# Optimization experiments

Hardware: AMD Instinct MI355X
Metric: run time of the kernel (lower is better)

The kernel has to match this reference:

```python
import jax, jax.numpy as jnp
from jax import lax
import numpy as np

N_VOX = 50000
B = 2
D, H, W = 8, 160, 160
CIN = 16
G = 3
K = 27
CHANS = [(16, 16), (16, 32), (32, 64), (64, 64), (64, 128)]
NAMES = ['in', 'e1', 'e2', 'e3', 'out']


def setup_inputs() -> dict:
    key = jax.random.key(0)
    ks = jax.random.split(key, 16)
    rng = np.random.default_rng(0)
    # unique active cells -> deterministic scatter/gather rulebook
    lin = rng.choice(B * D * H * W, size=N_VOX, replace=False)
    bz = lin // (D * H * W)
    rem = lin % (D * H * W)
    zz = rem // (H * W)
    yy = (rem % (H * W)) // W
    xx = rem % W
    coors = jnp.asarray(np.stack([bz, zz, yy, xx], 1).astype(np.int32))
    inp = {
        'voxel_features': jax.random.normal(ks[0], (N_VOX, CIN), jnp.float32),
        'coors': coors,
        'batch_size': B,
    }
    i = 1
    for nm, (ci, co) in zip(NAMES, CHANS):
        k1, k2 = jax.random.split(ks[i]); i += 1
        inp['wb_' + nm] = jax.random.normal(k1, (K, ci, co), jnp.float32) * 0.05
        inp['ws_' + nm] = jax.random.normal(k2, (K, ci, G, co), jnp.float32) * 0.05
        inp['gm_' + nm] = jnp.ones((co,), jnp.float32)
        inp['bt_' + nm] = jnp.zeros((co,), jnp.float32)
    return inp


def _kan_block(feat, nbr, wb, ws, gm, bt, centers, inv_h):
    # submanifold KAN conv: gather -> (silu base + RBF spline basis) GEMM -> accumulate
    n = feat.shape[0]
    fp = jnp.concatenate([feat, jnp.zeros((1, feat.shape[1]), feat.dtype)], 0)  # pad row for out-of-grid

    def body(acc, kin):
        idx, wbk, wsk = kin
        x = fp[idx]                                   # [N, Cin] gathered neighbors
        base = jax.nn.silu(x) @ wbk                   # [N, Cout]
        bas = jnp.exp(-jnp.square((x[:, :, None] - centers) * inv_h))  # [N, Cin, G]
        spl = jnp.einsum('ncg,cgo->no', bas, wsk)     # [N, Cout]
        return acc + base + spl, None

    out0 = jnp.zeros((n, wb.shape[-1]), feat.dtype)
    out, _ = lax.scan(jax.checkpoint(body), out0, (nbr, wb, ws))
    # BatchNorm1d (train-mode batch stats) + ReLU
    mu = out.mean(0)
    var = out.var(0)
    out = (out - mu) * lax.rsqrt(var + 1e-3) * gm + bt
    return jax.nn.relu(out)


def _build_rulebook(coors, batch_size, n):
    grid = jnp.full((batch_size, D + 2, H + 2, W + 2), n, jnp.int32)
    grid = grid.at[coors[:, 0], coors[:, 1] + 1, coors[:, 2] + 1, coors[:, 3] + 1].set(
        jnp.arange(n, dtype=jnp.int32))
    offs = [(dz, dy, dx) for dz in (-1, 0, 1) for dy in (-1, 0, 1) for dx in (-1, 0, 1)]
    return jnp.stack([
        grid[coors[:, 0], coors[:, 1] + 1 + dz, coors[:, 2] + 1 + dy, coors[:, 3] + 1 + dx]
        for dz, dy, dx in offs])  # [27, N]


def reference(voxel_features, coors, batch_size,
              wb_in, ws_in, gm_in, bt_in,
              wb_e1, ws_e1, gm_e1, bt_e1,
              wb_e2, ws_e2, gm_e2, bt_e2,
              wb_e3, ws_e3, gm_e3, bt_e3,
              wb_out, ws_out, gm_out, bt_out):
    n = voxel_features.shape[0]
    nbr = _build_rulebook(coors, batch_size, n)
    centers = jnp.linspace(-1.0, 1.0, G)
    inv_h = (G - 1) / 2.0
    x = _kan_block(voxel_features, nbr, wb_in, ws_in, gm_in, bt_in, centers, inv_h)
    x = _kan_block(x, nbr, wb_e1, ws_e1, gm_e1, bt_e1, centers, inv_h)
    x = _kan_block(x, nbr, wb_e2, ws_e2, gm_e2, bt_e2, centers, inv_h)
    x = _kan_block(x, nbr, wb_e3, ws_e3, gm_e3, bt_e3, centers, inv_h)
    x = _kan_block(x, nbr, wb_out, ws_out, gm_out, bt_out, centers, inv_h)
    co = x.shape[1]
    dense = jnp.zeros((batch_size, D, H, W, co), x.dtype)
    dense = dense.at[coors[:, 0], coors[:, 1], coors[:, 2], coors[:, 3]].set(x)
    dense = dense.transpose(0, 4, 1, 2, 3)            # [B, C, D, H, W]
    return dense.reshape(batch_size, co * D, H, W)    # [B, C*D, H, W]
```

## Files before the change

### kernel.cpp

```cpp
#include <hip/hip_runtime.h>

#define N_VOX 50000
#define BATCH 2
#define DD 8
#define HH 160
#define WW 160
#define PD 10
#define PH 162
#define PW 162
#define KK 27
#define NCELL (BATCH*DD*HH*WW)
#define GRID_ELEMS (BATCH*PD*PH*PW)
#define OUT_ELEMS (BATCH*128*DD*HH*WW)

typedef __attribute__((ext_vector_type(8))) short short8v;
typedef __attribute__((ext_vector_type(4))) float float4v;

__device__ inline unsigned short f2bf(float f) {
    unsigned u = __float_as_uint(f);
    u += 0x7FFFu + ((u >> 16) & 1u);
    return (unsigned short)(u >> 16);
}

__global__ void k_flags(const int* __restrict__ coors, int* __restrict__ flags) {
    int n = blockIdx.x * 256 + threadIdx.x;
    if (n >= N_VOX) return;
    int b = coors[n*4+0], z = coors[n*4+1], y = coors[n*4+2], x = coors[n*4+3];
    flags[((b*DD + z)*HH + y)*WW + x] = 1;
}

__global__ void k_scan1(const int* __restrict__ flags, int* __restrict__ scanout,
                        int* __restrict__ bsums) {
    __shared__ int s[256];
    int t = threadIdx.x, blk = blockIdx.x;
    int4 v = ((const int4*)(flags + blk*1024))[t];
    int tsum = v.x + v.y + v.z + v.w;
    s[t] = tsum; __syncthreads();
    for (int off = 1; off < 256; off <<= 1) {
        int x = (t >= off) ? s[t-off] : 0;
        __syncthreads(); s[t] += x; __syncthreads();
    }
    int excl = s[t] - tsum;
    int4 o; o.x = excl; o.y = excl + v.x; o.z = o.y + v.y; o.w = o.z + v.z;
    ((int4*)(scanout + blk*1024))[t] = o;
    if (t == 255) bsums[blk] = s[255];
}

__global__ void k_scan2(int* __restrict__ bsums) {
    __shared__ int s[512];
    int t = threadIdx.x;
    int orig = (t < 400) ? bsums[t] : 0;
    s[t] = orig; __syncthreads();
    for (int off = 1; off < 512; off <<= 1) {
        int x = (t >= off) ? s[t-off] : 0;
        __syncthreads(); s[t] += x; __syncthreads();
    }
    if (t < 400) bsums[t] = s[t] - orig;
}

__global__ void k_pos(const int* __restrict__ coors, const int* __restrict__ scanout,
                      const int* __restrict__ bsums, int* __restrict__ pos_of,
                      int* __restrict__ vox_at) {
    int n = blockIdx.x * 256 + threadIdx.x;
    if (n >= N_VOX) return;
    int b = coors[n*4+0], z = coors[n*4+1], y = coors[n*4+2], x = coors[n*4+3];
    int lin = ((b*DD + z)*HH + y)*WW + x;
    int pos = scanout[lin] + bsums[lin >> 10];
    pos_of[n] = pos;
    vox_at[pos] = n;
}

__global__ void k_gridP(const int* __restrict__ coors, const int* __restrict__ pos_of,
                        int* __restrict__ gridP) {
    int n = blockIdx.x * 256 + threadIdx.x;
    if (n >= N_VOX) return;
    int b = coors[n*4+0], z = coors[n*4+1], y = coors[n*4+2], x = coors[n*4+3];
    gridP[((b*PD + z+1)*PH + (y+1))*PW + (x+1)] = pos_of[n];
}

__global__ void k_nbrP(const int* __restrict__ coors, const int* __restrict__ vox_at,
                       const int* __restrict__ gridP, int* __restrict__ nbrP) {
    int i = blockIdx.x * 256 + threadIdx.x;
    if (i >= N_VOX) return;
    int n = vox_at[i];
    int b = coors[n*4+0], z = coors[n*4+1]+1, y = coors[n*4+2]+1, x = coors[n*4+3]+1;
    int k = 0;
    for (int dz = -1; dz <= 1; ++dz)
        for (int dy = -1; dy <= 1; ++dy)
            for (int dx = -1; dx <= 1; ++dx) {
                int g = gridP[((b*PD + z+dz)*PH + (y+dy))*PW + (x+dx)];
                nbrP[k*N_VOX + i] = (g >= 0) ? g : N_VOX;
                ++k;
            }
}

__global__ void k_phi0(const float* __restrict__ vf, const int* __restrict__ vox_at,
                       unsigned short* __restrict__ phi) {
    int e = blockIdx.x * 256 + threadIdx.x;
    if (e >= (N_VOX + 1) * 16) return;
    int i = e / 16, c = e % 16;
    float x = 0.f;
    if (i < N_VOX) x = vf[(size_t)vox_at[i] * 16 + c];
    float sig = 1.f / (1.f + __expf(-x));
    ushort4 p;
    p.x = f2bf(x * sig);
    p.y = f2bf(__expf(-(x + 1.f) * (x + 1.f)));
    p.z = f2bf(__expf(-x * x));
    p.w = f2bf(__expf(-(x - 1.f) * (x - 1.f)));
    *(ushort4*)&phi[(size_t)e * 4] = p;
}

struct WswzArgs {
    const float* wb[5];
    const float* ws[5];
    unsigned short* dst[5];
};
__global__ void k_wswz_all(WswzArgs a) {
    constexpr int off[6]   = {0, 27648, 82944, 304128, 746496, 1631232};
    constexpr int lgCI4[5] = {6, 6, 7, 8, 8};
    constexpr int lgCO[5]  = {4, 5, 6, 6, 7};
    int e = blockIdx.x * 256 + threadIdx.x;
    if (e >= off[5]) return;
    int L = 0;
    #pragma unroll
    for (int i = 1; i < 5; ++i) L += (e >= off[i]);
    int el = e - off[L];
    int CIN4 = 1 << lgCI4[L], COUT = 1 << lgCO[L], CIN = CIN4 >> 2;
    int j8   = el & 7;
    int rest = el >> 3;
    int o    = rest & (COUT - 1);
    int kb   = rest >> lgCO[L];
    int kabs = kb * 8 + j8;
    int k  = kabs >> lgCI4[L];
    int c4 = kabs & (CIN4 - 1);
    int c = c4 >> 2, jj = c4 & 3;
    float v = (jj == 0) ? a.wb[L][(k * CIN + c) * COUT + o]
                        : a.ws[L][((k * CIN + c) * 3 + (jj - 1)) * COUT + o];
    a.dst[L][el] = f2bf(v);
}

template<int CIN, int COUT, int NSPL>
__global__ __launch_bounds__(256) void k_conv_mfma(
    const unsigned short* __restrict__ phi,
    const int*            __restrict__ nbrP,
    const unsigned short* __restrict__ Wsw,
    float*                __restrict__ pre,
    float*                __restrict__ sums)
{
    constexpr int CIN4   = CIN * 4;
    constexpr int BK     = 64;
    constexpr int SPK    = CIN4 / BK;
    constexpr int NSTAGE = KK * SPK;
    constexpr int COUTH  = COUT / NSPL;
    constexpr int NFW    = COUTH / 16;
    constexpr int NMB    = (N_VOX + 127) / 128;
    constexpr int NBLK   = NMB * NSPL;
    constexpr int PERX   = (NBLK + 7) / 8;

    int lb = blockIdx.x;
    int linear = (lb & 7) * PERX + (lb >> 3);
    if (linear >= NBLK) return;
    const int mb = linear / NSPL, h = linear % NSPL;

    const int t = threadIdx.x, lane = t & 63, wv = t >> 6;
    const int l15 = lane & 15, q = lane >> 4;
    const int base = mb * 128;
    const int vg0 = base + wv * 32 + l15, vg1 = vg0 + 16;
    const int ob = h * COUTH;

    const unsigned short* bp = Wsw + (size_t)(q * COUT + ob + l15) * 8;

    int rows[2], rowsN[2];
    short8v A0[2][2], A1[2][2];
    short8v B0[2][NFW], B1[2][NFW];

    auto loadB = [&](int sp, short8v (&Bb)[2][NFW]) {
        #pragma unroll
        for (int kk = 0; kk < 2; ++kk)
            #pragma unroll
            for (int nf = 0; nf < NFW; ++nf)
                Bb[kk][nf] = *(const short8v*)(bp +
                    ((size_t)(sp * 8 + kk * 4) * COUT + nf * 16) * 8);
    };
    auto loadA = [&](int sp, short8v (&Ab)[2][2]) {
        if (sp % SPK == 0) { rows[0] = rowsN[0]; rows[1] = rowsN[1]; }
        const int c4s = (sp % SPK) * BK;
        const unsigned short* p0 = phi + (size_t)rows[0] * CIN4 + c4s + q * 8;
        const unsigned short* p1 = phi + (size_t)rows[1] * CIN4 + c4s + q * 8;
        Ab[0][0] = *(const short8v*)p0;        Ab[0][1] = *(const short8v*)p1;
        Ab[1][0] = *(const short8v*)(p0 + 32); Ab[1][1] = *(const short8v*)(p1 + 32);
        if (sp % SPK == 0) {
            int k2 = sp / SPK + 1;
            if (k2 < KK) {
                rowsN[0] = (vg0 < N_VOX) ? nbrP[k2 * N_VOX + vg0] : N_VOX;
                rowsN[1] = (vg1 < N_VOX) ? nbrP[k2 * N_VOX + vg1] : N_VOX;
            }
        }
    };

    float4v acc[2][NFW];
    #pragma unroll
    for (int mi = 0; mi < 2; ++mi)
        #pragma unroll
        for (int nf = 0; nf < NFW; ++nf)
            acc[mi][nf] = (float4v){0.f, 0.f, 0.f, 0.f};

    auto domfma = [&](const short8v (&Ab)[2][2], const short8v (&Bb)[2][NFW]) {
        #pragma unroll
        for (int kk = 0; kk < 2; ++kk)
            #pragma unroll
            for (int nf = 0; nf < NFW; ++nf) {
                acc[0][nf] = __builtin_amdgcn_mfma_f32_16x16x32_bf16(Ab[kk][0], Bb[kk][nf], acc[0][nf], 0, 0, 0);
                acc[1][nf] = __builtin_amdgcn_mfma_f32_16x16x32_bf16(Ab[kk][1], Bb[kk][nf], acc[1][nf], 0, 0, 0);
            }
    };

    rows[0]  = (vg0 < N_VOX) ? nbrP[vg0] : N_VOX;
    rows[1]  = (vg1 < N_VOX) ? nbrP[vg1] : N_VOX;
    rowsN[0] = (vg0 < N_VOX) ? nbrP[N_VOX + vg0] : N_VOX;
    rowsN[1] = (vg1 < N_VOX) ? nbrP[N_VOX + vg1] : N_VOX;
    loadB(0, B0);
    {
        const unsigned short* p0 = phi + (size_t)rows[0] * CIN4 + q * 8;
        const unsigned short* p1 = phi + (size_t)rows[1] * CIN4 + q * 8;
        A0[0][0] = *(const short8v*)p0;        A0[0][1] = *(const short8v*)p1;
        A0[1][0] = *(const short8v*)(p0 + 32); A0[1][1] = *(const short8v*)(p1 + 32);
    }

    int s = 0;
    for (; s + 2 <= NSTAGE; s += 2) {
        loadB(s + 1, B1); loadA(s + 1, A1);
        __builtin_amdgcn_sched_barrier(0);
        domfma(A0, B0);
        if (s + 2 < NSTAGE) { loadB(s + 2, B0); loadA(s + 2, A0); }
        __builtin_amdgcn_sched_barrier(0);
        domfma(A1, B1);
    }
    if (s < NSTAGE) domfma(A0, B0);

    #pragma unroll
    for (int mi = 0; mi < 2; ++mi)
        #pragma unroll
        for (int nf = 0; nf < NFW; ++nf)
            #pragma unroll
            for (int r = 0; r < 4; ++r) {
                int v = base + wv * 32 + mi * 16 + q * 4 + r;
                if (v < N_VOX)
                    pre[(size_t)v * COUT + ob + nf * 16 + l15] = acc[mi][nf][r];
            }

    float* S = sums + (blockIdx.x & 7) * 256;
    #pragma unroll
    for (int nf = 0; nf < NFW; ++nf) {
        float s1 = 0.f, s2 = 0.f;
        #pragma unroll
        for (int mi = 0; mi < 2; ++mi)
            #pragma unroll
            for (int r = 0; r < 4; ++r) {
                int v = base + wv * 32 + mi * 16 + q * 4 + r;
                if (v < N_VOX) {
                    float a = acc[mi][nf][r];
                    s1 += a; s2 += a * a;
                }
            }
        s1 += __shfl_xor(s1, 16); s1 += __shfl_xor(s1, 32);
        s2 += __shfl_xor(s2, 16); s2 += __shfl_xor(s2, 32);
        if (q == 0) {
            atomicAdd(&S[ob + nf * 16 + l15], s1);
            atomicAdd(&S[COUT + ob + nf * 16 + l15], s2);
        }
    }
}

template<int COUT>
__global__ void k_bnapply_phi(const float* __restrict__ pre, const float* __restrict__ sums,
                              const float* __restrict__ gm, const float* __restrict__ bt,
                              unsigned short* __restrict__ phi) {
    __shared__ float sc[COUT], sh[COUT];
    int t = threadIdx.x;
    if (t < COUT) {
        float s1 = 0.f, s2 = 0.f;
        #pragma unroll
        for (int xo = 0; xo < 8; ++xo) {
            s1 += sums[xo * 256 + t];
            s2 += sums[xo * 256 + COUT + t];
        }
        float mu  = s1 * (1.f / N_VOX);
        float var = s2 * (1.f / N_VOX) - mu*mu;
        float s = rsqrtf(var + 1e-3f) * gm[t];
        sc[t] = s;
        sh[t] = bt[t] - mu * s;
    }
    __syncthreads();
    int tot = (N_VOX + 1) * COUT;
    for (int e = blockIdx.x*256 + t; e < tot; e += gridDim.x*256) {
        int i = e / COUT, c = e % COUT;
        float x = 0.f;
        if (i < N_VOX) x = fmaxf(pre[(size_t)i*COUT + c] * sc[c] + sh[c], 0.f);
        float sig = 1.f / (1.f + __expf(-x));
        ushort4 p;
        p.x = f2bf(x * sig);
        p.y = f2bf(__expf(-(x + 1.f) * (x + 1.f)));
        p.z = f2bf(__expf(-x * x));
        p.w = f2bf(__expf(-(x - 1.f) * (x - 1.f)));
        *(ushort4*)&phi[(size_t)e * 4] = p;
    }
}

template<int COUT>
__global__ void k_bnapply_f32(float* __restrict__ pre, const float* __restrict__ sums,
                              const float* __restrict__ gm, const float* __restrict__ bt) {
    __shared__ float sc[COUT], sh[COUT];
    int t = threadIdx.x;
    if (t < COUT) {
        float s1 = 0.f, s2 = 0.f;
        #pragma unroll
        for (int xo = 0; xo < 8; ++xo) {
            s1 += sums[xo * 256 + t];
            s2 += sums[xo * 256 + COUT + t];
        }
        float mu  = s1 * (1.f / N_VOX);
        float var = s2 * (1.f / N_VOX) - mu*mu;
        float s = rsqrtf(var + 1e-3f) * gm[t];
        sc[t] = s;
        sh[t] = bt[t] - mu * s;
    }
    __syncthreads();
    for (int e = blockIdx.x*256 + t; e < N_VOX*COUT; e += gridDim.x*256) {
        int c = e % COUT;
        pre[e] = fmaxf(pre[e] * sc[c] + sh[c], 0.f);
    }
}

__global__ void k_dense(const float* __restrict__ feat, const int* __restrict__ gridP,
                        float* __restrict__ out) {
    int e4 = blockIdx.x*256 + threadIdx.x;
    if (e4 >= OUT_ELEMS/4) return;
    int e = e4 * 4;
    int x  = e % WW;
    int y  = (e / WW) % HH;
    int cz = (e / (WW*HH)) % (128*DD);
    int b  = e / (WW*HH*128*DD);
    int c = cz >> 3, z = cz & 7;
    const int* gp = &gridP[((b*PD + z+1)*PH + (y+1))*PW + (x+1)];
    int g0 = gp[0], g1 = gp[1], g2 = gp[2], g3 = gp[3];
    float4 o;
    o.x = (g0 >= 0) ? feat[(size_t)g0*128 + c] : 0.f;
    o.y = (g1 >= 0) ? feat[(size_t)g1*128 + c] : 0.f;
    o.z = (g2 >= 0) ? feat[(size_t)g2*128 + c] : 0.f;
    o.w = (g3 >= 0) ? feat[(size_t)g3*128 + c] : 0.f;
    *(float4*)&out[e] = o;
}

template<int CIN, int COUT, int NSPL>
static void run_block(const float* gm, const float* bt,
                      const int* nbrP, unsigned short* phi, const unsigned short* Wsw,
                      float* sums, float* pre, bool last, hipStream_t stream) {
    constexpr int NMB  = (N_VOX + 127) / 128;
    constexpr int NBLK = NMB * NSPL;
    constexpr int GRID = ((NBLK + 7) / 8) * 8;
    k_conv_mfma<CIN, COUT, NSPL><<<GRID, 256, 0, stream>>>(phi, nbrP, Wsw, pre, sums);
    if (last) {
        k_bnapply_f32<COUT><<<512, 256, 0, stream>>>(pre, sums, gm, bt);
    } else {
        k_bnapply_phi<COUT><<<512, 256, 0, stream>>>(pre, sums, gm, bt, phi);
    }
}

extern "C" void kernel_launch(void* const* d_in, const int* in_sizes, int n_in,
                              void* d_out, int out_size, void* d_ws, size_t ws_size,
                              hipStream_t stream) {
    const float* vf    = (const float*)d_in[0];
    const int*   coors = (const int*)d_in[1];
    const float* wb[5] = {(const float*)d_in[3],  (const float*)d_in[7],
                          (const float*)d_in[11], (const float*)d_in[15],
                          (const float*)d_in[19]};
    const float* wsp[5]= {(const float*)d_in[4],  (const float*)d_in[8],
                          (const float*)d_in[12], (const float*)d_in[16],
                          (const float*)d_in[20]};
    const float* gm[5] = {(const float*)d_in[5],  (const float*)d_in[9],
                          (const float*)d_in[13], (const float*)d_in[17],
                          (const float*)d_in[21]};
    const float* bt[5] = {(const float*)d_in[6],  (const float*)d_in[10],
                          (const float*)d_in[14], (const float*)d_in[18],
                          (const float*)d_in[22]};

    char* p = (char*)d_ws;
    auto alloc = [&](size_t bytes) {
        char* r = p;
        p += (bytes + 255) & ~(size_t)255;
        return r;
    };
    int*            flags   = (int*)           alloc((size_t)NCELL * 4);
    int*            scanout = (int*)           alloc((size_t)NCELL * 4);
    int*            bsums   = (int*)           alloc(512 * 4);
    int*            pos_of  = (int*)           alloc((size_t)N_VOX * 4);
    int*            vox_at  = (int*)           alloc((size_t)N_VOX * 4);
    int*            gridP   = (int*)           alloc((size_t)GRID_ELEMS * 4);
    int*            nbrP    = (int*)           alloc((size_t)KK * N_VOX * 4);
    unsigned short* Wsw0    = (unsigned short*)alloc((size_t)KK * 64  * 16  * 2);
    unsigned short* Wsw1    = (unsigned short*)alloc((size_t)KK * 64  * 32  * 2);
    unsigned short* Wsw2    = (unsigned short*)alloc((size_t)KK * 128 * 64  * 2);
    unsigned short* Wsw3    = (unsigned short*)alloc((size_t)KK * 256 * 64  * 2);
    unsigned short* Wsw4    = (unsigned short*)alloc((size_t)KK * 256 * 128 * 2);
    unsigned short* phi     = (unsigned short*)alloc((size_t)(N_VOX + 1) * 256 * 2);
    float*          sumsAll = (float*)         alloc(5 * 8 * 256 * 4);
    float*          pre     = (float*)         alloc((size_t)N_VOX * 128 * 4);

    hipMemsetAsync(flags, 0, (size_t)NCELL * 4, stream);
    hipMemsetAsync(gridP, 0xFF, (size_t)GRID_ELEMS * 4, stream);
    hipMemsetAsync(sumsAll, 0, 5 * 8 * 256 * 4, stream);

    WswzArgs wa;
    for (int i = 0; i < 5; ++i) { wa.wb[i] = wb[i]; wa.ws[i] = wsp[i]; }
    wa.dst[0] = Wsw0; wa.dst[1] = Wsw1; wa.dst[2] = Wsw2; wa.dst[3] = Wsw3; wa.dst[4] = Wsw4;
    k_wswz_all<<<(1631232 + 255) / 256, 256, 0, stream>>>(wa);

    k_flags<<<(N_VOX+255)/256, 256, 0, stream>>>(coors, flags);
    k_scan1<<<NCELL/1024, 256, 0, stream>>>(flags, scanout, bsums);
    k_scan2<<<1, 512, 0, stream>>>(bsums);
    k_pos  <<<(N_VOX+255)/256, 256, 0, stream>>>(coors, scanout, bsums, pos_of, vox_at);
    k_gridP<<<(N_VOX+255)/256, 256, 0, stream>>>(coors, pos_of, gridP);
    k_nbrP <<<(N_VOX+255)/256, 256, 0, stream>>>(coors, vox_at, gridP, nbrP);
    {
        int n = (N_VOX + 1) * 16;
        k_phi0<<<(n + 255) / 256, 256, 0, stream>>>(vf, vox_at, phi);
    }

    run_block<16, 16,  1>(gm[0], bt[0], nbrP, phi, Wsw0, sumsAll + 0*2048, pre, false, stream);
    run_block<16, 32,  1>(gm[1], bt[1], nbrP, phi, Wsw1, sumsAll + 1*2048, pre, false, stream);
    run_block<32, 64,  1>(gm[2], bt[2], nbrP, phi, Wsw2, sumsAll + 2*2048, pre, false, stream);
    run_block<64, 64,  1>(gm[3], bt[3], nbrP, phi, Wsw3, sumsAll + 3*2048, pre, false, stream);
    run_block<64, 128, 2>(gm[4], bt[4], nbrP, phi, Wsw4, sumsAll + 4*2048, pre, true,  stream);

    k_dense<<<(OUT_ELEMS/4 + 255)/256, 256, 0, stream>>>(pre, gridP, (float*)d_out);
}
```

Measured before the change: 736.8 us.

## Triple-buffer A gathers with two-stage lookahead and split output channels

The MFMA conv main loop rotates three A-operand register buffers so that neighbour-row gathers are issued two stages ahead of use, and neighbour indices are prefetched two kernel offsets ahead. This is meant to hide the latency of the irregular gather loads behind more MFMA work. Separately, layers e1–e3 now split output channels across two blocks, which doubles the grid for more parallelism but re-gathers the same A rows once per half. The extra buffers raise register pressure and may lower occupancy.

```diff
diff --git a/kernel.cpp b/kernel.cpp
--- a/kernel.cpp
+++ b/kernel.cpp
@@ -151,6 +151,7 @@
     constexpr int BK     = 64;
     constexpr int SPK    = CIN4 / BK;
     constexpr int NSTAGE = KK * SPK;
+    static_assert(NSTAGE % 3 == 0, "3-slot rotation needs NSTAGE % 3 == 0");
     constexpr int COUTH  = COUT / NSPL;
     constexpr int NFW    = COUTH / 16;
     constexpr int NMB    = (N_VOX + 127) / 128;
@@ -170,8 +171,8 @@
 
     const unsigned short* bp = Wsw + (size_t)(q * COUT + ob + l15) * 8;
 
-    int rows[2], rowsN[2];
-    short8v A0[2][2], A1[2][2];
+    int rows[2], rowsN[2], rowsN2[2];
+    short8v A0[2][2], A1[2][2], A2[2][2];
     short8v B0[2][NFW], B1[2][NFW];
 
     auto loadB = [&](int sp, short8v (&Bb)[2][NFW]) {
@@ -183,17 +184,20 @@
                     ((size_t)(sp * 8 + kk * 4) * COUT + nf * 16) * 8);
     };
     auto loadA = [&](int sp, short8v (&Ab)[2][2]) {
-        if (sp % SPK == 0) { rows[0] = rowsN[0]; rows[1] = rowsN[1]; }
+        if (sp % SPK == 0) {
+            rows[0]  = rowsN[0];  rows[1]  = rowsN[1];
+            rowsN[0] = rowsN2[0]; rowsN[1] = rowsN2[1];
+        }
         const int c4s = (sp % SPK) * BK;
         const unsigned short* p0 = phi + (size_t)rows[0] * CIN4 + c4s + q * 8;
         const unsigned short* p1 = phi + (size_t)rows[1] * CIN4 + c4s + q * 8;
         Ab[0][0] = *(const short8v*)p0;        Ab[0][1] = *(const short8v*)p1;
         Ab[1][0] = *(const short8v*)(p0 + 32); Ab[1][1] = *(const short8v*)(p1 + 32);
         if (sp % SPK == 0) {
-            int k2 = sp / SPK + 1;
+            int k2 = sp / SPK + 2;
             if (k2 < KK) {
-                rowsN[0] = (vg0 < N_VOX) ? nbrP[k2 * N_VOX + vg0] : N_VOX;
-                rowsN[1] = (vg1 < N_VOX) ? nbrP[k2 * N_VOX + vg1] : N_VOX;
+                rowsN2[0] = (vg0 < N_VOX) ? nbrP[k2 * N_VOX + vg0] : N_VOX;
+                rowsN2[1] = (vg1 < N_VOX) ? nbrP[k2 * N_VOX + vg1] : N_VOX;
             }
         }
     };
@@ -215,10 +219,12 @@
             }
     };
 
-    rows[0]  = (vg0 < N_VOX) ? nbrP[vg0] : N_VOX;
-    rows[1]  = (vg1 < N_VOX) ? nbrP[vg1] : N_VOX;
-    rowsN[0] = (vg0 < N_VOX) ? nbrP[N_VOX + vg0] : N_VOX;
-    rowsN[1] = (vg1 < N_VOX) ? nbrP[N_VOX + vg1] : N_VOX;
+    rows[0]   = (vg0 < N_VOX) ? nbrP[vg0] : N_VOX;
+    rows[1]   = (vg1 < N_VOX) ? nbrP[vg1] : N_VOX;
+    rowsN[0]  = (vg0 < N_VOX) ? nbrP[N_VOX + vg0] : N_VOX;
+    rowsN[1]  = (vg1 < N_VOX) ? nbrP[N_VOX + vg1] : N_VOX;
+    rowsN2[0] = (vg0 < N_VOX) ? nbrP[2 * N_VOX + vg0] : N_VOX;
+    rowsN2[1] = (vg1 < N_VOX) ? nbrP[2 * N_VOX + vg1] : N_VOX;
     loadB(0, B0);
     {
         const unsigned short* p0 = phi + (size_t)rows[0] * CIN4 + q * 8;
@@ -226,17 +232,30 @@
         A0[0][0] = *(const short8v*)p0;        A0[0][1] = *(const short8v*)p1;
         A0[1][0] = *(const short8v*)(p0 + 32); A0[1][1] = *(const short8v*)(p1 + 32);
     }
+    loadB(1, B1);
+    loadA(1, A1);
+
+    #define SLOT(T, Ac, Bc, An, Bn)                                   \
+        if ((T) + 2 < NSTAGE) loadA((T) + 2, An);                     \
+        if ((T) + 1 < NSTAGE) loadB((T) + 1, Bn);                     \
+        __builtin_amdgcn_sched_barrier(0);                            \
+        domfma(Ac, Bc);
 
     int s = 0;
-    for (; s + 2 <= NSTAGE; s += 2) {
-        loadB(s + 1, B1); loadA(s + 1, A1);
-        __builtin_amdgcn_sched_barrier(0);
-        domfma(A0, B0);
-        if (s + 2 < NSTAGE) { loadB(s + 2, B0); loadA(s + 2, A0); }
-        __builtin_amdgcn_sched_barrier(0);
-        domfma(A1, B1);
-    }
-    if (s < NSTAGE) domfma(A0, B0);
+    for (; s + 6 <= NSTAGE; s += 6) {
+        SLOT(s + 0, A0, B0, A2, B1)
+        SLOT(s + 1, A1, B1, A0, B0)
+        SLOT(s + 2, A2, B0, A1, B1)
+        SLOT(s + 3, A0, B1, A2, B0)
+        SLOT(s + 4, A1, B0, A0, B1)
+        SLOT(s + 5, A2, B1, A1, B0)
+    }
+    if constexpr (NSTAGE % 6 != 0) {
+        SLOT(s + 0, A0, B0, A2, B1)
+        SLOT(s + 1, A1, B1, A0, B0)
+        SLOT(s + 2, A2, B0, A1, B1)
+    }
+    #undef SLOT
 
     #pragma unroll
     for (int mi = 0; mi < 2; ++mi)
@@ -428,9 +447,9 @@
     }
 
     run_block<16, 16,  1>(gm[0], bt[0], nbrP, phi, Wsw0, sumsAll + 0*2048, pre, false, stream);
-    run_block<16, 32,  1>(gm[1], bt[1], nbrP, phi, Wsw1, sumsAll + 1*2048, pre, false, stream);
-    run_block<32, 64,  1>(gm[2], bt[2], nbrP, phi, Wsw2, sumsAll + 2*2048, pre, false, stream);
-    run_block<64, 64,  1>(gm[3], bt[3], nbrP, phi, Wsw3, sumsAll + 3*2048, pre, false, stream);
+    run_block<16, 32,  2>(gm[1], bt[1], nbrP, phi, Wsw1, sumsAll + 1*2048, pre, false, stream);
+    run_block<32, 64,  2>(gm[2], bt[2], nbrP, phi, Wsw2, sumsAll + 2*2048, pre, false, stream);
+    run_block<64, 64,  2>(gm[3], bt[3], nbrP, phi, Wsw3, sumsAll + 3*2048, pre, false, stream);
     run_block<64, 128, 2>(gm[4], bt[4], nbrP, phi, Wsw4, sumsAll + 4*2048, pre, true,  stream);
 
     k_dense<<<(OUT_ELEMS/4 + 255)/256, 256, 0, stream>>>(pre, gridP, (float*)d_out);
```

Result: slower. 797.9 us (+8.3%).

## Use single-wave blocks covering 64 voxels to reuse B fragments across rows

Applied to the files above, without the earlier changes.

Switches the conv kernel from 256-thread blocks where each wave handles 32 voxels to 64-thread blocks where one wave handles 64 voxels (four 16-row tiles). Each loaded weight fragment now feeds four MFMAs instead of two, which halves B-fragment global loads per output and raises MFMA density per load. In exchange each wave holds more accumulator and A registers, which can lower occupancy. The kernel also issues more, smaller blocks and twice as many per-block atomic adds for the batch-norm sums.

```diff
diff --git a/kernel.cpp b/kernel.cpp
--- a/kernel.cpp
+++ b/kernel.cpp
@@ -140,7 +140,7 @@
 }
 
 template<int CIN, int COUT, int NSPL>
-__global__ __launch_bounds__(256) void k_conv_mfma(
+__global__ __launch_bounds__(64, 2) void k_conv_mfma(
     const unsigned short* __restrict__ phi,
     const int*            __restrict__ nbrP,
     const unsigned short* __restrict__ Wsw,
@@ -153,7 +153,8 @@
     constexpr int NSTAGE = KK * SPK;
     constexpr int COUTH  = COUT / NSPL;
     constexpr int NFW    = COUTH / 16;
-    constexpr int NMB    = (N_VOX + 127) / 128;
+    constexpr int WR     = 4;
+    constexpr int NMB    = (N_VOX + 63) / 64;
     constexpr int NBLK   = NMB * NSPL;
     constexpr int PERX   = (NBLK + 7) / 8;
 
@@ -162,16 +163,18 @@
     if (linear >= NBLK) return;
     const int mb = linear / NSPL, h = linear % NSPL;
 
-    const int t = threadIdx.x, lane = t & 63, wv = t >> 6;
+    const int lane = threadIdx.x & 63;
     const int l15 = lane & 15, q = lane >> 4;
-    const int base = mb * 128;
-    const int vg0 = base + wv * 32 + l15, vg1 = vg0 + 16;
+    const int base = mb * 64;
+    int vg[WR];
+    #pragma unroll
+    for (int rs = 0; rs < WR; ++rs) vg[rs] = base + rs * 16 + l15;
     const int ob = h * COUTH;
 
     const unsigned short* bp = Wsw + (size_t)(q * COUT + ob + l15) * 8;
 
-    int rows[2], rowsN[2];
-    short8v A0[2][2], A1[2][2];
+    int rows[WR], rowsN[WR];
+    short8v A0[2][WR], A1[2][WR];
     short8v B0[2][NFW], B1[2][NFW];
 
     auto loadB = [&](int sp, short8v (&Bb)[2][NFW]) {
@@ -182,71 +185,83 @@
                 Bb[kk][nf] = *(const short8v*)(bp +
                     ((size_t)(sp * 8 + kk * 4) * COUT + nf * 16) * 8);
     };
-    auto loadA = [&](int sp, short8v (&Ab)[2][2]) {
-        if (sp % SPK == 0) { rows[0] = rowsN[0]; rows[1] = rowsN[1]; }
+    auto loadA = [&](int sp, short8v (&Ab)[2][WR]) {
+        if (sp % SPK == 0) {
+            #pragma unroll
+            for (int rs = 0; rs < WR; ++rs) rows[rs] = rowsN[rs];
+        }
         const int c4s = (sp % SPK) * BK;
-        const unsigned short* p0 = phi + (size_t)rows[0] * CIN4 + c4s + q * 8;
-        const unsigned short* p1 = phi + (size_t)rows[1] * CIN4 + c4s + q * 8;
-        Ab[0][0] = *(const short8v*)p0;        Ab[0][1] = *(const short8v*)p1;
-        Ab[1][0] = *(const short8v*)(p0 + 32); Ab[1][1] = *(const short8v*)(p1 + 32);
+        #pragma unroll
+        for (int rs = 0; rs < WR; ++rs) {
+            const unsigned short* p = phi + (size_t)rows[rs] * CIN4 + c4s + q * 8;
+            Ab[0][rs] = *(const short8v*)p;
+            Ab[1][rs] = *(const short8v*)(p + 32);
+        }
         if (sp % SPK == 0) {
             int k2 = sp / SPK + 1;
             if (k2 < KK) {
-                rowsN[0] = (vg0 < N_VOX) ? nbrP[k2 * N_VOX + vg0] : N_VOX;
-                rowsN[1] = (vg1 < N_VOX) ? nbrP[k2 * N_VOX + vg1] : N_VOX;
+                #pragma unroll
+                for (int rs = 0; rs < WR; ++rs)
+                    rowsN[rs] = (vg[rs] < N_VOX) ? nbrP[k2 * N_VOX + vg[rs]] : N_VOX;
             }
         }
     };
 
-    float4v acc[2][NFW];
-    #pragma unroll
-    for (int mi = 0; mi < 2; ++mi)
+    float4v acc[WR][NFW];
+    #pragma unroll
+    for (int rs = 0; rs < WR; ++rs)
         #pragma unroll
         for (int nf = 0; nf < NFW; ++nf)
-            acc[mi][nf] = (float4v){0.f, 0.f, 0.f, 0.f};
-
-    auto domfma = [&](const short8v (&Ab)[2][2], const short8v (&Bb)[2][NFW]) {
+            acc[rs][nf] = (float4v){0.f, 0.f, 0.f, 0.f};
+
+    auto domfma = [&](const short8v (&Ab)[2][WR], const short8v (&Bb)[2][NFW]) {
         #pragma unroll
         for (int kk = 0; kk < 2; ++kk)
             #pragma unroll
-            for (int nf = 0; nf < NFW; ++nf) {
-                acc[0][nf] = __builtin_amdgcn_mfma_f32_16x16x32_bf16(Ab[kk][0], Bb[kk][nf], acc[0][nf], 0, 0, 0);
-                acc[1][nf] = __builtin_amdgcn_mfma_f32_16x16x32_bf16(Ab[kk][1], Bb[kk][nf], acc[1][nf], 0, 0, 0);
-            }
+            for (int nf = 0; nf < NFW; ++nf)
+                #pragma unroll
+                for (int rs = 0; rs < WR; ++rs)
+                    acc[rs][nf] = __builtin_amdgcn_mfma_f32_16x16x32_bf16(
+                        Ab[kk][rs], Bb[kk][nf], acc[rs][nf], 0, 0, 0);
     };
 
-    rows[0]  = (vg0 < N_VOX) ? nbrP[vg0] : N_VOX;
-    rows[1]  = (vg1 < N_VOX) ? nbrP[vg1] : N_VOX;
-    rowsN[0] = (vg0 < N_VOX) ? nbrP[N_VOX + vg0] : N_VOX;
-    rowsN[1] = (vg1 < N_VOX) ? nbrP[N_VOX + vg1] : N_VOX;
+    #pragma unroll
+    for (int rs = 0; rs < WR; ++rs) {
+        rows[rs]  = (vg[rs] < N_VOX) ? nbrP[vg[rs]] : N_VOX;
+        rowsN[rs] = (vg[rs] < N_VOX) ? nbrP[N_VOX + vg[rs]] : N_VOX;
+    }
     loadB(0, B0);
-    {
-        const unsigned short* p0 = phi + (size_t)rows[0] * CIN4 + q * 8;
-        const unsigned short* p1 = phi + (size_t)rows[1] * CIN4 + q * 8;
-        A0[0][0] = *(const short8v*)p0;        A0[0][1] = *(const short8v*)p1;
-        A0[1][0] = *(const short8v*)(p0 + 32); A0[1][1] = *(const short8v*)(p1 + 32);
-    }
+    #pragma unroll
+    for (int rs = 0; rs < WR; ++rs) {
+        const unsigned short* p = phi + (size_t)rows[rs] * CIN4 + q * 8;
+        A0[0][rs] = *(const short8v*)p;
+        A0[1][rs] = *(const short8v*)(p + 32);
+    }
+
+    #define SLOT(T, Ac, Bc, An, Bn)                                   \
+        if ((T) + 1 < NSTAGE) { loadB((T) + 1, Bn); loadA((T) + 1, An); } \
+        __builtin_amdgcn_sched_barrier(0);                            \
+        domfma(Ac, Bc);
 
     int s = 0;
     for (; s + 2 <= NSTAGE; s += 2) {
-        loadB(s + 1, B1); loadA(s + 1, A1);
-        __builtin_amdgcn_sched_barrier(0);
+        SLOT(s + 0, A0, B0, A1, B1)
+        SLOT(s + 1, A1, B1, A0, B0)
+    }
+    if constexpr (NSTAGE % 2 != 0) {
         domfma(A0, B0);
-        if (s + 2 < NSTAGE) { loadB(s + 2, B0); loadA(s + 2, A0); }
-        __builtin_amdgcn_sched_barrier(0);
-        domfma(A1, B1);
-    }
-    if (s < NSTAGE) domfma(A0, B0);
-
-    #pragma unroll
-    for (int mi = 0; mi < 2; ++mi)
+    }
+    #undef SLOT
+
+    #pragma unroll
+    for (int rs = 0; rs < WR; ++rs)
         #pragma unroll
         for (int nf = 0; nf < NFW; ++nf)
             #pragma unroll
             for (int r = 0; r < 4; ++r) {
-                int v = base + wv * 32 + mi * 16 + q * 4 + r;
+                int v = base + rs * 16 + q * 4 + r;
                 if (v < N_VOX)
-                    pre[(size_t)v * COUT + ob + nf * 16 + l15] = acc[mi][nf][r];
+                    pre[(size_t)v * COUT + ob + nf * 16 + l15] = acc[rs][nf][r];
             }
 
     float* S = sums + (blockIdx.x & 7) * 256;
@@ -254,12 +269,12 @@
     for (int nf = 0; nf < NFW; ++nf) {
         float s1 = 0.f, s2 = 0.f;
         #pragma unroll
-        for (int mi = 0; mi < 2; ++mi)
+        for (int rs = 0; rs < WR; ++rs)
             #pragma unroll
             for (int r = 0; r < 4; ++r) {
-                int v = base + wv * 32 + mi * 16 + q * 4 + r;
+                int v = base + rs * 16 + q * 4 + r;
                 if (v < N_VOX) {
-                    float a = acc[mi][nf][r];
+                    float a = acc[rs][nf][r];
                     s1 += a; s2 += a * a;
                 }
             }
@@ -356,10 +371,10 @@
 static void run_block(const float* gm, const float* bt,
                       const int* nbrP, unsigned short* phi, const unsigned short* Wsw,
                       float* sums, float* pre, bool last, hipStream_t stream) {
-    constexpr int NMB  = (N_VOX + 127) / 128;
+    constexpr int NMB  = (N_VOX + 63) / 64;
     constexpr int NBLK = NMB * NSPL;
     constexpr int GRID = ((NBLK + 7) / 8) * 8;
-    k_conv_mfma<CIN, COUT, NSPL><<<GRID, 256, 0, stream>>>(phi, nbrP, Wsw, pre, sums);
+    k_conv_mfma<CIN, COUT, NSPL><<<GRID, 64, 0, stream>>>(phi, nbrP, Wsw, pre, sums);
     if (last) {
         k_bnapply_f32<COUT><<<512, 256, 0, stream>>>(pre, sums, gm, bt);
     } else {
```

After: 661.8 us. -10.2%, faster.
